# Performance work log

Measured on AMD Instinct MI355X. Metric: run time of the kernel, lower is better.

## Reference

```python
import jax, jax.numpy as jnp
import numpy as np

BATCH = 8
N_CLASSES = 3            # including background
PRE_NMS_LIMIT = 6000
NMS_THRESH = 0.5
SCALE = 512.0
WINDOW = (0.0, 0.0, 512.0, 512.0)   # y1, x1, y2, x2
STD_DEV = np.array([0.1, 0.1, 0.2, 0.2], np.float32)
GROUP_OFFSET = 4096.0    # > image extent; separates (batch, class) groups in NMS

_RATIOS = np.array([0.5, 1.0, 2.0])
_LEVELS = [((128, 128), 4, 8.0), ((64, 64), 8, 16.0), ((32, 32), 16, 32.0), ((16, 16), 32, 64.0)]


def _gen_anchors():
    # faithful port of generate_pyramid_anchors / generate_anchors (anchor_stride=1)
    out = []
    for (fy, fx), stride, scale in _LEVELS:
        s, r = np.meshgrid(np.array([scale]), _RATIOS)
        s, r = s.flatten(), r.flatten()
        heights = s / np.sqrt(r)
        widths = s * np.sqrt(r)
        sy = np.arange(fy) * stride
        sx = np.arange(fx) * stride
        sx, sy = np.meshgrid(sx, sy)
        bw, bcx = np.meshgrid(widths, sx)
        bh, bcy = np.meshgrid(heights, sy)
        centers = np.stack([bcy, bcx], axis=2).reshape(-1, 2)
        sizes = np.stack([bh, bw], axis=2).reshape(-1, 2)
        out.append(np.concatenate([centers - 0.5 * sizes, centers + 0.5 * sizes], axis=1))
    return np.concatenate(out, axis=0).astype(np.float32)  # (65280, 4) yxyx


def setup_inputs() -> dict:
    key = jax.random.key(0)
    k1, k2 = jax.random.split(key)
    anchors = jnp.asarray(_gen_anchors())
    n_anchors = anchors.shape[0]
    n_prop = BATCH * n_anchors
    logits = jax.random.normal(k1, (n_prop, N_CLASSES), jnp.float32)
    probs = jax.nn.softmax(logits, axis=-1)
    deltas = jax.random.normal(k2, (n_prop, 4), jnp.float32)
    batch_ixs = jnp.repeat(jnp.arange(BATCH, dtype=jnp.int64), n_anchors)
    return {"probs": probs, "deltas": deltas, "anchors": anchors, "batch_ixs": batch_ixs}


def _apply_box_deltas_2d(boxes, deltas):
    # boxes: (K,4) yxyx (normalized); deltas: (K,4) dy,dx,dh,dw
    h = boxes[:, 2] - boxes[:, 0]
    w = boxes[:, 3] - boxes[:, 1]
    cy = boxes[:, 0] + 0.5 * h + deltas[:, 0] * h
    cx = boxes[:, 1] + 0.5 * w + deltas[:, 1] * w
    h = h * jnp.exp(deltas[:, 2])
    w = w * jnp.exp(deltas[:, 3])
    y1 = cy - 0.5 * h
    x1 = cx - 0.5 * w
    return jnp.stack([y1, x1, y1 + h, x1 + w], axis=1)


def _nms_keep(boxes, thresh):
    # boxes (K,4), already sorted by score descending; returns bool keep mask.
    y1, x1, y2, x2 = boxes[:, 0], boxes[:, 1], boxes[:, 2], boxes[:, 3]
    areas = (y2 - y1 + 1.0) * (x2 - x1 + 1.0)
    ih = jnp.clip(jnp.minimum(y2[:, None], y2[None, :]) - jnp.maximum(y1[:, None], y1[None, :]) + 1.0, 0.0)
    iw = jnp.clip(jnp.minimum(x2[:, None], x2[None, :]) - jnp.maximum(x1[:, None], x1[None, :]) + 1.0, 0.0)
    inter = ih * iw
    iou = inter / (areas[:, None] + areas[None, :] - inter)  # (K,K)
    K = boxes.shape[0]
    idx = jnp.arange(K)

    def body(i, keep):
        sup = (iou[i] >= thresh) & (idx > i) & keep[i]
        return keep & ~sup

    return jax.lax.fori_loop(0, K, body, jnp.ones((K,), bool))


def reference(probs, deltas, anchors, batch_ixs):
    n_anchors = anchors.shape[0]
    n_fg = probs.shape[1] - 1
    # trim to top pre_nms_limit foreground scores (flat over proposals x fg classes)
    fg = probs[:, 1:].reshape(-1)
    scores, flat_ix = jax.lax.top_k(fg, PRE_NMS_LIMIT)  # sorted descending
    prop_ix = flat_ix // n_fg
    class_ids = flat_ix % n_fg + 1
    b = batch_ixs[prop_ix]
    a = anchors[prop_ix % n_anchors]        # anchors tiled per batch element
    d = deltas[prop_ix] * jnp.asarray(STD_DEV)
    rois = _apply_box_deltas_2d(a / SCALE, d) * SCALE
    lo = jnp.array([WINDOW[0], WINDOW[1], WINDOW[0], WINDOW[1]], rois.dtype)
    hi = jnp.array([WINDOW[2], WINDOW[3], WINDOW[2], WINDOW[3]], rois.dtype)
    rois = jnp.clip(rois, lo, hi)
    # batched per-class NMS: offset boxes so different (batch, class) groups never overlap
    group = (b * (n_fg + 1) + class_ids).astype(rois.dtype) * GROUP_OFFSET
    keep = _nms_keep(rois + group[:, None], NMS_THRESH)
    detections = jnp.concatenate(
        [rois, scores[:, None], keep.astype(rois.dtype)[:, None]], axis=1)  # (K, 6)
    return detections, class_ids, b
```

## Files before the change

kernel.cpp:

```cpp
#include <hip/hip_runtime.h>
#include <math.h>

typedef unsigned int u32;
typedef unsigned short u16;
typedef unsigned long long u64;

#define PRE_NMS 6000
#define NBLK    94
#define KMAX    640
#define MSTRIDE 11
#define MAXW    10
#define MTILE   (MAXW * MAXW)
#define FINEB   8192
#define LOWB    8064
#define NHB     128
#define CANDMAX 16384
#define NGRP    24
#define FLOOR_BITS 0x3F000000u

#define CTR_OFF    0
#define FINEH_OFF  256
#define BCNT_OFF   33024
#define GBITS_OFF  98560
#define ZERO_LEN   116992
#define CAND_OFF   116992
#define BOXR_OFF   248064
#define KG_OFF     344320
#define GRANKG_OFF 344576
#define BOXG_OFF   406016
#define AREAG_OFF  651776
#define MASKG_OFF  713216
#define BASE_OFF   2064896
#define PART_OFF   2130432

__device__ __forceinline__ u32 bucket_of(u32 bits) {
    if (bits >= FLOOR_BITS) {
        u32 fb = (bits - FLOOR_BITS) >> 10; if (fb > FINEB - 1) fb = FINEB - 1;
        return fb;
    }
    return 8192u + (bits >> 17);
}

__global__ __launch_bounds__(1024) void histpivot_kernel(const float4* __restrict__ probs4,
                                                         u32* __restrict__ fineh,
                                                         u32* __restrict__ partials,
                                                         u32* __restrict__ ctr,
                                                         u32* __restrict__ base,
                                                         int n_prop) {
    __shared__ u32 hf[FINEB];
    __shared__ u32 hl[2][LOWB];
    __shared__ u32 s_tick;
    int t = threadIdx.x;
    for (int i = t; i < FINEB; i += 1024) hf[i] = 0u;
    for (int i = t; i < 2 * LOWB; i += 1024) ((u32*)hl)[i] = 0u;
    __syncthreads();
    u32* l = hl[(t >> 6) & 1];
    int nq = n_prop >> 2;
    int idx = blockIdx.x * 1024 + t;
    int stride = gridDim.x * 1024;
    for (int q = idx; q < nq; q += stride) {
        float4 a = probs4[3 * q + 0];
        float4 b = probs4[3 * q + 1];
        float4 c = probs4[3 * q + 2];
        float vs[8] = {a.y, a.z, b.x, b.y, b.w, c.x, c.z, c.w};
        #pragma unroll
        for (int e = 0; e < 8; ++e) {
            u32 bits = __float_as_uint(vs[e]);
            if (bits >= FLOOR_BITS) {
                u32 fb = (bits - FLOOR_BITS) >> 10; if (fb >= FINEB) fb = FINEB - 1;
                atomicAdd(&hf[fb], 1u);
            } else {
                atomicAdd(&l[bits >> 17], 1u);
            }
        }
    }
    __syncthreads();
    for (int b = t; b < FINEB; b += 1024) {
        u32 v = hf[b];
        if (v) atomicAdd(&fineh[b], v);
    }
    u32* outp = partials + blockIdx.x * LOWB;
    for (int b = t; b < LOWB; b += 1024) outp[b] = hl[0][b] + hl[1][b];
    __syncthreads();

    if (t == 0) {
        __threadfence();
        s_tick = atomicAdd(&ctr[2], 1u);
    }
    __syncthreads();
    if (s_tick != (u32)gridDim.x - 1u) return;

    __threadfence();
    u32* fh = hf;
    u32* sd = hl[0];
    for (int b = t; b < FINEB; b += 1024) fh[b] = fineh[b];
    __syncthreads();
    int hi = FINEB - 1 - 8 * t;
    u32 L = 0;
    #pragma unroll
    for (int e = 0; e < 8; ++e) L += fh[hi - e];
    sd[t] = L;
    __syncthreads();
    for (int off = 1; off < 1024; off <<= 1) {
        u32 x = (t >= off) ? sd[t - off] : 0u;
        __syncthreads();
        sd[t] += x;
        __syncthreads();
    }
    u32 incl = sd[t], excl = incl - L;
    u32 fineTotal = sd[1023];
    {
        u32 run = excl;
        #pragma unroll
        for (int e = 0; e < 8; ++e) {
            int fb = hi - e;
            base[fb] = run;
            u32 c = fh[fb];
            if (run < (u32)PRE_NMS && run + c >= (u32)PRE_NMS) {
                ctr[1] = FLOOR_BITS + ((u32)fb << 10);
                u32 m = run + c; if (m > (u32)CANDMAX) m = (u32)CANDMAX;
                ctr[0] = m;
            }
            run += c;
        }
    }
    if (fineTotal >= (u32)PRE_NMS) return;

    u32 rem = (u32)PRE_NMS - fineTotal;
    __syncthreads();
    for (int b = t; b < FINEB; b += 1024) {
        u32 s = 0;
        if (b < LOWB) {
            for (int k = 0; k < NHB; ++k) s += partials[k * LOWB + b];
        }
        fh[b] = s;
    }
    __syncthreads();
    L = 0;
    #pragma unroll
    for (int e = 0; e < 8; ++e) L += fh[hi - e];
    sd[t] = L;
    __syncthreads();
    for (int off = 1; off < 1024; off <<= 1) {
        u32 x = (t >= off) ? sd[t - off] : 0u;
        __syncthreads();
        sd[t] += x;
        __syncthreads();
    }
    incl = sd[t]; excl = incl - L;
    {
        u32 run = excl;
        #pragma unroll
        for (int e = 0; e < 8; ++e) {
            int lb = hi - e;
            base[8192 + lb] = fineTotal + run;
            u32 c = fh[lb];
            if (run < rem && run + c >= rem) {
                ctr[1] = ((u32)lb) << 17;
                u32 m = fineTotal + run + c; if (m > (u32)CANDMAX) m = (u32)CANDMAX;
                ctr[0] = m;
            }
            run += c;
        }
    }
}

__global__ __launch_bounds__(256) void scatter_kernel(const float4* __restrict__ probs4,
                                                      const u32* __restrict__ ctr,
                                                      const u32* __restrict__ base,
                                                      u32* __restrict__ bcnt,
                                                      u64* __restrict__ cand,
                                                      int n_prop) {
    u32 pivot = ctr[1];
    int nq = n_prop >> 2;
    int idx = blockIdx.x * 256 + threadIdx.x;
    int stride = gridDim.x * 256;
    for (int q = idx; q < nq; q += stride) {
        float4 a = probs4[3 * q + 0];
        float4 b = probs4[3 * q + 1];
        float4 c = probs4[3 * q + 2];
        float vs[8] = {a.y, a.z, b.x, b.y, b.w, c.x, c.z, c.w};
        #pragma unroll
        for (int e = 0; e < 8; ++e) {
            u32 bits = __float_as_uint(vs[e]);
            if (bits >= pivot) {
                u32 bk = bucket_of(bits);
                u32 off = atomicAdd(&bcnt[bk], 1u);
                u32 slot = base[bk] + off;
                u32 i = (u32)(8 * q + e);
                if (slot < (u32)CANDMAX) cand[slot] = ((u64)bits << 32) | (u64)(~i);
            }
        }
    }
}

__global__ __launch_bounds__(256) void rankdecode_kernel(const u64* __restrict__ cand,
                                                         const u32* __restrict__ ctr,
                                                         const u32* __restrict__ base,
                                                         const u32* __restrict__ bcnt,
                                                         const float4* __restrict__ deltas4,
                                                         const float4* __restrict__ anchors4,
                                                         float4* __restrict__ boxr,
                                                         u32* __restrict__ gbits,
                                                         float* __restrict__ out,
                                                         int n_anch) {
    u32 M = ctr[0]; if (M > (u32)CANDMAX) M = (u32)CANDMAX;
    u32 i = blockIdx.x * 256 + threadIdx.x;
    if (i >= M) return;
    u64 key = cand[i];
    u32 bits = (u32)(key >> 32);
    u32 bk = bucket_of(bits);
    u32 b0 = base[bk];
    u32 n = bcnt[bk];
    u32 r = b0;
    if (n > 1) {
        u32 end = b0 + n; if (end > M) end = M;
        u32 cnt = 0;
        for (u32 j = b0; j < end; ++j) cnt += (cand[j] > key) ? 1u : 0u;
        r = b0 + cnt;
    }
    if (r >= (u32)PRE_NMS) return;
    u32 flat = ~((u32)key);
    int p = (int)(flat >> 1);
    int cls = (int)(flat & 1u) + 1;
    int b = p / n_anch;
    int g = b * 3 + cls;
    int aidx = p - b * n_anch;
    float score = __uint_as_float(bits);
    float4 a = anchors4[aidx];
    float4 d = deltas4[p];
    float d0 = d.x * 0.1f, d1 = d.y * 0.1f, d2 = d.z * 0.2f, d3 = d.w * 0.2f;
    float y1 = a.x * (1.0f / 512.0f), x1 = a.y * (1.0f / 512.0f);
    float y2 = a.z * (1.0f / 512.0f), x2 = a.w * (1.0f / 512.0f);
    float h = y2 - y1, w = x2 - x1;
    float cy = y1 + 0.5f * h + d0 * h;
    float cx = x1 + 0.5f * w + d1 * w;
    h = h * expf(d2);
    w = w * expf(d3);
    float ry1 = (cy - 0.5f * h) * 512.0f;
    float rx1 = (cx - 0.5f * w) * 512.0f;
    float ry2 = (cy - 0.5f * h + h) * 512.0f;
    float rx2 = (cx - 0.5f * w + w) * 512.0f;
    ry1 = fminf(fmaxf(ry1, 0.0f), 512.0f);
    rx1 = fminf(fmaxf(rx1, 0.0f), 512.0f);
    ry2 = fminf(fmaxf(ry2, 0.0f), 512.0f);
    rx2 = fminf(fmaxf(rx2, 0.0f), 512.0f);
    out[r * 6 + 0] = ry1;
    out[r * 6 + 1] = rx1;
    out[r * 6 + 2] = ry2;
    out[r * 6 + 3] = rx2;
    out[r * 6 + 4] = score;
    out[r * 6 + 5] = 1.0f;
    out[PRE_NMS * 6 + r] = (float)cls;
    out[PRE_NMS * 7 + r] = (float)b;
    boxr[r] = make_float4(ry1, rx1, ry2, rx2);
    atomicOr(&gbits[g * 192 + (r >> 5)], 1u << (r & 31));
}

__global__ __launch_bounds__(512) void prep_kernel(const u32* __restrict__ gbits,
                                                   const float4* __restrict__ boxr,
                                                   u32* __restrict__ kg,
                                                   u32* __restrict__ grankg,
                                                   float4* __restrict__ boxg,
                                                   float* __restrict__ areag) {
    __shared__ int bpre[96];
    __shared__ u16 grankS[KMAX];
    __shared__ int sK;
    int g = blockIdx.x, t = threadIdx.x, lane = t & 63, wv = t >> 6;
    const u32* rb32 = gbits + g * 192;

    if (t < 64) {
        u64 w0 = (u64)rb32[2 * lane] | ((u64)rb32[2 * lane + 1] << 32);
        u64 w1 = (lane < NBLK - 64)
                 ? ((u64)rb32[128 + 2 * lane] | ((u64)rb32[129 + 2 * lane] << 32)) : 0ull;
        int c0 = (int)__popcll(w0), c1 = (int)__popcll(w1);
        int i0 = c0, i1 = c1;
        #pragma unroll
        for (int off = 1; off < 64; off <<= 1) {
            int a = __shfl_up(i0, off); if (lane >= off) i0 += a;
            int b = __shfl_up(i1, off); if (lane >= off) i1 += b;
        }
        int tot0 = __shfl(i0, 63), tot1 = __shfl(i1, 63);
        bpre[lane] = i0 - c0;
        if (lane < 32) bpre[64 + lane] = tot0 + ((lane < NBLK - 64) ? (i1 - c1) : 0);
        if (lane == 0) { sK = tot0 + tot1; kg[g] = (u32)(tot0 + tot1); }
    }
    __syncthreads();
    int K = sK;
    if (K == 0) return;
    int Kc = (K < KMAX) ? K : KMAX;

    for (int blk = wv; blk < NBLK; blk += 8) {
        u64 wmask = (u64)rb32[2 * blk] | ((u64)rb32[2 * blk + 1] << 32);
        if ((wmask >> lane) & 1ull) {
            int pos = bpre[blk] + (int)__popcll(wmask & ((1ull << lane) - 1ull));
            if (pos < KMAX) grankS[pos] = (u16)((blk << 6) | lane);
        }
    }
    __syncthreads();

    float4* bg = boxg + g * KMAX;
    float*  ag = areag + g * KMAX;
    u32*    gr = grankg + g * KMAX;
    for (int m = t; m < KMAX; m += 512) {
        if (m < Kc) {
            int r = grankS[m];
            float4 bb = boxr[r];
            bg[m] = bb;
            ag[m] = (bb.z - bb.x + 1.0f) * (bb.w - bb.y + 1.0f);
            gr[m] = (u32)r;
        } else {
            bg[m] = make_float4(-3e30f, -3e30f, -3e30f, -3e30f);
            ag[m] = 3e38f;
        }
    }
}

__global__ __launch_bounds__(64) void mask_kernel(const u32* __restrict__ kg,
                                                  const float4* __restrict__ boxg,
                                                  const float* __restrict__ areag,
                                                  u64* __restrict__ maskg) {
    int g = blockIdx.y;
    u32 K = kg[g];
    if (K == 0u) return;
    int Kc = (K < (u32)KMAX) ? (int)K : KMAX;
    int W = (Kc + 63) >> 6;
    int u = blockIdx.x;
    int c = u / MAXW, rbk = u % MAXW;
    if (c >= W || rbk >= W) return;
    int lane = threadIdx.x;
    int r = rbk * 64 + lane;
    u64* mg = maskg + (size_t)g * (KMAX * MSTRIDE);
    if (rbk > c) { mg[r * MSTRIDE + c] = 0ull; return; }
    int j0 = c << 6;
    const float4* bg = boxg + g * KMAX;
    const float*  ag = areag + g * KMAX;
    float4 rb = bg[r];
    float  ra = ag[r];
    float4 cb = bg[j0 + lane];
    float  ca = ag[j0 + lane];
    u64 word = 0ull;
    #pragma unroll 8
    for (int q = 0; q < 64; ++q) {
        float cbx = __shfl(cb.x, q);
        float cby = __shfl(cb.y, q);
        float cbz = __shfl(cb.z, q);
        float cbw = __shfl(cb.w, q);
        float cav = __shfl(ca, q);
        float ih = fminf(rb.z, cbz) - fmaxf(rb.x, cbx) + 1.0f;
        float iw = fminf(rb.w, cbw) - fmaxf(rb.y, cby) + 1.0f;
        ih = fmaxf(ih, 0.0f); iw = fmaxf(iw, 0.0f);
        bool o = (3.0f * ih * iw >= ra + cav) && ((j0 + q) > r);
        if (o) word |= (1ull << q);
    }
    mg[r * MSTRIDE + c] = word;
}

__global__ __launch_bounds__(512) void greedy_kernel(const u32* __restrict__ kg,
                                                     const u32* __restrict__ grankg,
                                                     const u64* __restrict__ maskg,
                                                     float* __restrict__ out) {
    __shared__ u64 maskm[KMAX * MSTRIDE + 64];
    __shared__ u16 grank[KMAX];
    int g = blockIdx.x, t = threadIdx.x, lane = t & 63;
    u32 K = kg[g];
    if (K == 0u) return;
    int Kc = (K < (u32)KMAX) ? (int)K : KMAX;
    int W = (Kc + 63) >> 6;
    const u64* mg = maskg + (size_t)g * (KMAX * MSTRIDE);
    int nw = Kc * MSTRIDE;
    for (int m = t; m < nw; m += 512) maskm[m] = mg[m];
    for (int m = nw + t; m < nw + 64; m += 512) maskm[m] = 0ull;
    for (int m = t; m < Kc; m += 512) grank[m] = (u16)grankg[g * KMAX + m];
    __syncthreads();

    if (t >= 64) return;
    u64 remv = 0ull;
    for (int w = 0; w < W; ++w) {
        int r0 = w << 6;
        int rend = Kc - r0; if (rend > 64) rend = 64;
        u64 curw = __shfl(remv, w);
        u64 kb = 0ull;
        for (int b0 = 0; b0 < rend; b0 += 8) {
            int n = rend - b0; if (n > 8) n = 8;
            u64 mrow[8], dg[8];
            #pragma unroll
            for (int j = 0; j < 8; ++j) {
                int rr = r0 + b0 + ((j < n) ? j : 0);
                mrow[j] = maskm[rr * MSTRIDE + lane];
                dg[j]   = maskm[rr * MSTRIDE + w];
            }
            #pragma unroll
            for (int j = 0; j < 8; ++j) {
                if (j < n) {
                    int b = b0 + j;
                    u64 km = ((curw >> b) & 1ull) ? 0ull : ~0ull;
                    curw |= dg[j] & km;
                    remv |= mrow[j] & km;
                    kb |= km & (1ull << b);
                }
            }
        }
        if (lane < rend)
            out[(int)grank[r0 + lane] * 6 + 5] = ((kb >> lane) & 1ull) ? 1.0f : 0.0f;
    }
}

extern "C" void kernel_launch(void* const* d_in, const int* in_sizes, int n_in,
                              void* d_out, int out_size, void* d_ws, size_t ws_size,
                              hipStream_t stream) {
    const float*  probs    = (const float*)d_in[0];
    const float4* deltas4  = (const float4*)d_in[1];
    const float4* anchors4 = (const float4*)d_in[2];
    int n_prop = in_sizes[1] / 4;
    int n_anch = in_sizes[2] / 4;

    char* ws = (char*)d_ws;
    u32* ctr      = (u32*)(ws + CTR_OFF);
    u32* fineh    = (u32*)(ws + FINEH_OFF);
    u32* bcnt     = (u32*)(ws + BCNT_OFF);
    u32* gbits    = (u32*)(ws + GBITS_OFF);
    u64* cand     = (u64*)(ws + CAND_OFF);
    float4* boxr  = (float4*)(ws + BOXR_OFF);
    u32* kg       = (u32*)(ws + KG_OFF);
    u32* grankg   = (u32*)(ws + GRANKG_OFF);
    float4* boxg  = (float4*)(ws + BOXG_OFF);
    float* areag  = (float*)(ws + AREAG_OFF);
    u64* maskg    = (u64*)(ws + MASKG_OFF);
    u32* base     = (u32*)(ws + BASE_OFF);
    u32* partials = (u32*)(ws + PART_OFF);
    float* out    = (float*)d_out;

    hipMemsetAsync(ws, 0, ZERO_LEN, stream);
    histpivot_kernel<<<NHB, 1024, 0, stream>>>((const float4*)probs, fineh, partials,
                                               ctr, base, n_prop);
    scatter_kernel<<<512, 256, 0, stream>>>((const float4*)probs, ctr, base, bcnt,
                                            cand, n_prop);
    rankdecode_kernel<<<CANDMAX / 256, 256, 0, stream>>>(cand, ctr, base, bcnt,
                                                         deltas4, anchors4,
                                                         boxr, gbits, out, n_anch);
    prep_kernel<<<NGRP, 512, 0, stream>>>(gbits, boxr, kg, grankg, boxg, areag);
    mask_kernel<<<dim3(MTILE, NGRP), 64, 0, stream>>>(kg, boxg, areag, maskg);
    greedy_kernel<<<NGRP, 512, 0, stream>>>(kg, grankg, maskg, out);
}
```

Before: 145.0 us.

## Drop per-block low histograms; rescan probs in last block only on fallback

The histogram kernel no longer builds or writes per-block coarse histograms for scores below the fine floor. If the fine range turns out to hold fewer than the pre-NMS limit, the last block rescans all probabilities itself to build the low histogram. This removes shared-memory atomics and a global partials write and reduction from the common path, and frees shared memory. The rare fallback becomes a single-block full scan. Grid sizes for the histogram and scatter kernels are also halved.

```diff
diff --git a/kernel.cpp b/kernel.cpp
--- a/kernel.cpp
+++ b/kernel.cpp
@@ -13,7 +13,7 @@
 #define MTILE   (MAXW * MAXW)
 #define FINEB   8192
 #define LOWB    8064
-#define NHB     128
+#define NHB     64
 #define CANDMAX 16384
 #define NGRP    24
 #define FLOOR_BITS 0x3F000000u
@@ -31,7 +31,6 @@
 #define AREAG_OFF  651776
 #define MASKG_OFF  713216
 #define BASE_OFF   2064896
-#define PART_OFF   2130432
 
 __device__ __forceinline__ u32 bucket_of(u32 bits) {
     if (bits >= FLOOR_BITS) {
@@ -43,18 +42,16 @@
 
 __global__ __launch_bounds__(1024) void histpivot_kernel(const float4* __restrict__ probs4,
                                                          u32* __restrict__ fineh,
-                                                         u32* __restrict__ partials,
                                                          u32* __restrict__ ctr,
                                                          u32* __restrict__ base,
                                                          int n_prop) {
     __shared__ u32 hf[FINEB];
-    __shared__ u32 hl[2][LOWB];
+    __shared__ u32 sd[1024];
+    __shared__ u32 hlow[LOWB];
     __shared__ u32 s_tick;
     int t = threadIdx.x;
     for (int i = t; i < FINEB; i += 1024) hf[i] = 0u;
-    for (int i = t; i < 2 * LOWB; i += 1024) ((u32*)hl)[i] = 0u;
-    __syncthreads();
-    u32* l = hl[(t >> 6) & 1];
+    __syncthreads();
     int nq = n_prop >> 2;
     int idx = blockIdx.x * 1024 + t;
     int stride = gridDim.x * 1024;
@@ -69,8 +66,6 @@
             if (bits >= FLOOR_BITS) {
                 u32 fb = (bits - FLOOR_BITS) >> 10; if (fb >= FINEB) fb = FINEB - 1;
                 atomicAdd(&hf[fb], 1u);
-            } else {
-                atomicAdd(&l[bits >> 17], 1u);
             }
         }
     }
@@ -79,8 +74,6 @@
         u32 v = hf[b];
         if (v) atomicAdd(&fineh[b], v);
     }
-    u32* outp = partials + blockIdx.x * LOWB;
-    for (int b = t; b < LOWB; b += 1024) outp[b] = hl[0][b] + hl[1][b];
     __syncthreads();
 
     if (t == 0) {
@@ -92,7 +85,6 @@
 
     __threadfence();
     u32* fh = hf;
-    u32* sd = hl[0];
     for (int b = t; b < FINEB; b += 1024) fh[b] = fineh[b];
     __syncthreads();
     int hi = FINEB - 1 - 8 * t;
@@ -128,13 +120,21 @@
 
     u32 rem = (u32)PRE_NMS - fineTotal;
     __syncthreads();
-    for (int b = t; b < FINEB; b += 1024) {
-        u32 s = 0;
-        if (b < LOWB) {
-            for (int k = 0; k < NHB; ++k) s += partials[k * LOWB + b];
-        }
-        fh[b] = s;
-    }
+    for (int i = t; i < LOWB; i += 1024) hlow[i] = 0u;
+    __syncthreads();
+    for (int q = t; q < nq; q += 1024) {
+        float4 a = probs4[3 * q + 0];
+        float4 b = probs4[3 * q + 1];
+        float4 c = probs4[3 * q + 2];
+        float vs[8] = {a.y, a.z, b.x, b.y, b.w, c.x, c.z, c.w};
+        #pragma unroll
+        for (int e = 0; e < 8; ++e) {
+            u32 bits = __float_as_uint(vs[e]);
+            if (bits < FLOOR_BITS) atomicAdd(&hlow[bits >> 17], 1u);
+        }
+    }
+    __syncthreads();
+    for (int b = t; b < FINEB; b += 1024) fh[b] = (b < LOWB) ? hlow[b] : 0u;
     __syncthreads();
     L = 0;
     #pragma unroll
@@ -428,13 +428,12 @@
     float* areag  = (float*)(ws + AREAG_OFF);
     u64* maskg    = (u64*)(ws + MASKG_OFF);
     u32* base     = (u32*)(ws + BASE_OFF);
-    u32* partials = (u32*)(ws + PART_OFF);
     float* out    = (float*)d_out;
 
     hipMemsetAsync(ws, 0, ZERO_LEN, stream);
-    histpivot_kernel<<<NHB, 1024, 0, stream>>>((const float4*)probs, fineh, partials,
+    histpivot_kernel<<<NHB, 1024, 0, stream>>>((const float4*)probs, fineh,
                                                ctr, base, n_prop);
-    scatter_kernel<<<512, 256, 0, stream>>>((const float4*)probs, ctr, base, bcnt,
+    scatter_kernel<<<256, 256, 0, stream>>>((const float4*)probs, ctr, base, bcnt,
                                             cand, n_prop);
     rankdecode_kernel<<<CANDMAX / 256, 256, 0, stream>>>(cand, ctr, base, bcnt,
                                                          deltas4, anchors4,
```

Result: faster. 140.1 us (-3.4%).
